# Performance work log

Measured on AMD Instinct MI355X. Metric: run time of the kernel, lower is better.

## Reference

```python
import jax, jax.numpy as jnp
import numpy as np

SUBSET_CHANNELS = 128


def setup_inputs() -> dict:
    key = jax.random.key(0)
    k_in, k_q, k_k, k_v = jax.random.split(key, 4)
    B, S, C, D = 8, 2048, 1024, SUBSET_CHANNELS
    scale = 1.0 / np.sqrt(C)  # ~ default torch Linear init scale
    return {
        "input": jax.random.normal(k_in, (B, S, C), dtype=jnp.float32),
        "Wq": jax.random.normal(k_q, (C, D), dtype=jnp.float32) * scale,
        "Wk": jax.random.normal(k_k, (C, D), dtype=jnp.float32) * scale,
        "Wv": jax.random.normal(k_v, (C, D), dtype=jnp.float32) * scale,
    }


def reference(input, Wq, Wk, Wv):
    # Projections (bias=False): [B,S,C] @ [C,D] -> [B,S,D]
    Q = input @ Wq
    K = input @ Wk
    V = input @ Wv
    D = Wq.shape[1]
    # scores[b, i, j] = Q[b,i,:] . K[b,j,:], scaled by sqrt(subset_channels)
    scores = jnp.einsum("bqd,bkd->bqk", Q, K) / jnp.sqrt(jnp.asarray(D, Q.dtype))
    # NOTE: original applies softmax over dim=1 (the QUERY axis), non-standard.
    att = jax.nn.softmax(scores, axis=1)
    # output[b, i, :] = sum_j att[b,i,j] * V[b,j,:]
    return jnp.einsum("bqk,bkd->bqd", att, V)
```

## Files before the change

### kernel.cpp

```cpp
#include <hip/hip_runtime.h>
#include <hip/hip_bf16.h>

typedef __bf16 bf16_t;
typedef bf16_t bf16x4 __attribute__((ext_vector_type(4)));
typedef bf16_t bf16x8 __attribute__((ext_vector_type(8)));
typedef float f32x4 __attribute__((ext_vector_type(4)));
typedef __attribute__((address_space(1))) const unsigned int gu32_t;
typedef __attribute__((address_space(3))) unsigned int lu32_t;

#define MFMA(a, b, c) __builtin_amdgcn_mfma_f32_16x16x32_bf16(a, b, c, 0, 0, 0)

constexpr int B = 8, S = 2048, C = 1024, D = 128;
constexpr float C2 = 0.12751744f;


__global__ __launch_bounds__(256) void k_wt(const float* Wq, const float* Wk, const float* Wv, bf16_t* Wf) {
    int ct = blockIdx.x, w = blockIdx.y;
    const float* src = (w == 0) ? Wq : ((w == 1) ? Wk : Wv);
    __shared__ bf16_t tile[16][132];
    int t = threadIdx.x;
    int cr = t >> 4, dq = t & 15;
    const float* p = src + (size_t)(ct * 16 + cr) * D + dq * 8;
    f32x4 v0 = *(const f32x4*)p;
    f32x4 v1 = *(const f32x4*)(p + 4);
#pragma unroll
    for (int q = 0; q < 4; ++q) { tile[cr][dq * 8 + q] = (bf16_t)v0[q]; tile[cr][dq * 8 + 4 + q] = (bf16_t)v1[q]; }
    __syncthreads();
    int n = t >> 1, g = t & 1;
    bf16x8 o;
#pragma unroll
    for (int cc = 0; cc < 8; ++cc) o[cc] = tile[g * 8 + cc][n];
    int c8 = ct * 2 + g;
    int nblk = w * 8 + (n >> 4);
    size_t a = ((size_t)(nblk * 32 + (c8 >> 2)) * 64 + (c8 & 3) * 16 + (n & 15)) * 8;
    *(bf16x8*)(Wf + a) = o;
}

__global__ __launch_bounds__(512, 4) void k_qkv(const float* X, const bf16_t* Wf,
                                                bf16_t* Qf, bf16_t* Kf, float* Vf,
                                                float* Out) {
    __shared__ __align__(16) char pool_[65536];
    bf16_t* xfr = (bf16_t*)pool_;
    bf16_t* qkL = (bf16_t*)pool_;
    float*  vL  = (float*)(pool_ + 16896);
    int mt = blockIdx.x;
    int t = threadIdx.x;
    int lane = t & 63, wid = t >> 6;
    int lr = lane & 15, lg = lane >> 4;
    int rw = mt * 32;

    {
        f32x4* O4 = (f32x4*)Out;
        f32x4 z = {};
        int u = mt * 512 + t;
        __builtin_nontemporal_store(z, O4 + u);
        __builtin_nontemporal_store(z, O4 + u + 262144);
    }

    {
        f32x4 xa[8], xb[8];
#pragma unroll
        for (int p = 0; p < 8; ++p) {
            int fi = p * 8 + wid;
            int m = rw + (fi >> 5) * 16 + lr;
            int c = (fi & 31) * 32 + lg * 8;
            const f32x4* px = (const f32x4*)(X + (size_t)m * C + c);
            xa[p] = __builtin_nontemporal_load(px);
            xb[p] = __builtin_nontemporal_load(px + 1);
        }
#pragma unroll
        for (int p = 0; p < 8; ++p) {
            bf16x8 o;
#pragma unroll
            for (int q = 0; q < 4; ++q) { o[q] = (bf16_t)xa[p][q]; o[4 + q] = (bf16_t)xb[p][q]; }
            *(bf16x8*)&xfr[(size_t)(p * 8 + wid) * 512 + lane * 8] = o;
        }
    }

    f32x4 acc[2][3] = {};
    const bf16_t* wbase = Wf + (size_t)(wid * 3) * 32 * 512 + lane * 8;
    auto wld = [&](int nf, int kkg) {
        return *(const bf16x8*)(wbase + (size_t)(nf * 32 + kkg) * 512);
    };

    bf16x8 wr_[3][3];
#pragma unroll
    for (int d = 0; d < 3; ++d)
#pragma unroll
        for (int nf = 0; nf < 3; ++nf) wr_[d][nf] = wld(nf, d);
    __syncthreads();

#pragma unroll
    for (int kk = 0; kk < 32; ++kk) {
        int slot = kk % 3;
        bf16x8 a0 = *(const bf16x8*)&xfr[(size_t)kk * 512 + lane * 8];
        bf16x8 a1 = *(const bf16x8*)&xfr[(size_t)(32 + kk) * 512 + lane * 8];
        __builtin_amdgcn_s_setprio(1);
        acc[0][0] = MFMA(a0, wr_[slot][0], acc[0][0]);
        acc[1][0] = MFMA(a1, wr_[slot][0], acc[1][0]);
        acc[0][1] = MFMA(a0, wr_[slot][1], acc[0][1]);
        acc[1][1] = MFMA(a1, wr_[slot][1], acc[1][1]);
        acc[0][2] = MFMA(a0, wr_[slot][2], acc[0][2]);
        acc[1][2] = MFMA(a1, wr_[slot][2], acc[1][2]);
        __builtin_amdgcn_s_setprio(0);
        if (kk < 29) {
#pragma unroll
            for (int nf = 0; nf < 3; ++nf) wr_[slot][nf] = wld(nf, kk + 3);
        }
    }

    __syncthreads();
#pragma unroll
    for (int mi = 0; mi < 2; ++mi)
#pragma unroll
        for (int nf = 0; nf < 3; ++nf) {
            int n = wid * 48 + nf * 16 + lr;
            int sel = (wid * 48 + nf * 16) >> 7;
#pragma unroll
            for (int r = 0; r < 4; ++r) {
                int mloc = mi * 16 + lg * 4 + r;
                float v = acc[mi][nf][r];
                if (sel == 2) vL[mloc * 132 + (n - 256)] = v;
                else          qkL[mloc * 264 + n] = (bf16_t)v;
            }
        }
    __syncthreads();
#pragma unroll
    for (int p = 0; p < 2; ++p) {
        int F = wid * 2 + p;
        int isK = F >> 3, iblk = (F >> 2) & 1, dblk = F & 3;
        int m16 = lane & 15, kg = lane >> 4;
        int col = isK * 128 + dblk * 32 + kg * 8;
        bf16x8 o = *(const bf16x8*)&qkL[(iblk * 16 + m16) * 264 + col];
        bf16_t* dst = isK ? Kf : Qf;
        size_t frg = (size_t)((rw >> 4) + iblk) * 4 + dblk;
        __builtin_nontemporal_store(o, (bf16x8*)(dst + (frg * 64 + lane) * 8));
    }
#pragma unroll
    for (int p = 0; p < 2; ++p) {
        int u = p * 512 + t;
        int m = u >> 5, dq = u & 31;
        f32x4 v = *(const f32x4*)&vL[m * 132 + dq * 4];
        __builtin_nontemporal_store(v, (f32x4*)(Vf + (size_t)(rw + m) * D + dq * 4));
    }
}

__global__ __launch_bounds__(512, 4) void k_sum(const bf16_t* Qf, const bf16_t* Kf,
                                                const float* Vf, bf16_t* Vt2) {
    int l = blockIdx.x;
    int b = l & 7, jt = l >> 3;
    int j0 = jt * 32;
    int t = threadIdx.x;
    int lane = t & 63, wid = t >> 6;
    __shared__ __align__(16) bf16_t vtile[128 * 40];
    __shared__ float lsum[256];
    __shared__ float linv[32];

    bf16x8 kf[2][4];
    int jblkg = (b * S + j0) >> 4;
#pragma unroll
    for (int jF = 0; jF < 2; ++jF)
#pragma unroll
        for (int kk = 0; kk < 4; ++kk)
            kf[jF][kk] = *(const bf16x8*)(Kf + ((size_t)((jblkg + jF) * 4 + kk) * 64 + lane) * 8);

    float ls0 = 0.f, ls1 = 0.f;
#pragma unroll 4
    for (int tt = 0; tt < 16; ++tt) {
        int iblk = (b * S + wid * 256 + tt * 16) >> 4;
        bf16x8 qa[4];
#pragma unroll
        for (int kk = 0; kk < 4; ++kk)
            qa[kk] = *(const bf16x8*)(Qf + ((size_t)(iblk * 4 + kk) * 64 + lane) * 8);
        f32x4 s0 = {}, s1 = {};
#pragma unroll
        for (int kk = 0; kk < 4; ++kk) {
            s0 = MFMA(qa[kk], kf[0][kk], s0);
            s1 = MFMA(qa[kk], kf[1][kk], s1);
        }
#pragma unroll
        for (int r = 0; r < 4; ++r) { ls0 += exp2f(s0[r] * C2); ls1 += exp2f(s1[r] * C2); }
    }
    {
        float v0 = ls0 + __shfl_xor(ls0, 16); v0 += __shfl_xor(v0, 32);
        float v1 = ls1 + __shfl_xor(ls1, 16); v1 += __shfl_xor(v1, 32);
        if (lane < 16) { lsum[wid * 32 + lane] = v0; lsum[wid * 32 + 16 + lane] = v1; }
    }
    __syncthreads();
    if (t < 32) {
        float ss = 0.f;
#pragma unroll
        for (int w = 0; w < 8; ++w) ss += lsum[w * 32 + t];
        linv[t] = 1.0f / ss;
    }
    __syncthreads();
#pragma unroll
    for (int p = 0; p < 2; ++p) {
        int u = p * 512 + t;
        int jj = u & 31, dq = u >> 5;
        f32x4 v = *(const f32x4*)(Vf + (size_t)(b * S + j0 + jj) * D + dq * 4);
        float inv = linv[jj];
#pragma unroll
        for (int q = 0; q < 4; ++q)
            vtile[(dq * 4 + q) * 40 + jj] = (bf16_t)(v[q] * inv);
    }
    __syncthreads();
    {
        int d = t >> 2, jg = t & 3;
        bf16x8 row = *(const bf16x8*)&vtile[d * 40 + jg * 8];
        size_t j32g = (size_t)b * 64 + jt;
        size_t a = ((j32g * 8 + (d >> 4)) * 64 + jg * 16 + (d & 15)) * 8;
        *(bf16x8*)(Vt2 + a) = row;
    }
}

__global__ __launch_bounds__(512, 4) void k_out(const bf16_t* Qf, const bf16_t* Kf,
                                                const bf16_t* Vt2, float* Out) {
    int l = blockIdx.x;
    int b = l & 7, it = (l >> 3) & 31, jh = l >> 8;
    int ibase = it * 64;
    int t = threadIdx.x;
    int lane = t & 63, wid = t >> 6;
    int lr = lane & 15, lg = lane >> 4;
    int ig = wid >> 1, jq = wid & 1;
    __shared__ __align__(16) bf16_t pool[37888];
    bf16_t* klds = pool;
    bf16_t* vlds = pool + 16384;
    bf16_t* pl = pool + 32768 + wid * 640;

    bf16x8 qf[4];
    int iblk = (b * S + ibase + ig * 16) >> 4;
#pragma unroll
    for (int kk = 0; kk < 4; ++kk)
        qf[kk] = *(const bf16x8*)(Qf + ((size_t)(iblk * 4 + kk) * 64 + lane) * 8);

    f32x4 acc[8] = {};
    const bf16_t* kbase = Kf + (size_t)(b * S + jh * 1024) * 128 + wid * 1024 + lane * 8;
    const bf16_t* vbase = Vt2 + (size_t)(b * 64 + jh * 32) * 4096 + wid * 1024 + lane * 8;

    auto stageKV = [&](int bufi, int tt) {
        const bf16_t* gk = kbase + (size_t)tt * 8192;
        __builtin_amdgcn_global_load_lds((gu32_t*)gk, (lu32_t*)&klds[bufi * 8192 + wid * 1024], 16, 0, 0);
        __builtin_amdgcn_global_load_lds((gu32_t*)(gk + 512), (lu32_t*)&klds[bufi * 8192 + wid * 1024 + 512], 16, 0, 0);
        const bf16_t* gv = vbase + (size_t)tt * 8192;
        __builtin_amdgcn_global_load_lds((gu32_t*)gv, (lu32_t*)&vlds[bufi * 8192 + wid * 1024], 16, 0, 0);
        __builtin_amdgcn_global_load_lds((gu32_t*)(gv + 512), (lu32_t*)&vlds[bufi * 8192 + wid * 1024 + 512], 16, 0, 0);
    };
    stageKV(0, 0);
    __syncthreads();

    for (int tt = 0; tt < 16; ++tt) {
        int buf = tt & 1;
        if (tt < 15) stageKV(buf ^ 1, tt + 1);
#pragma unroll
        for (int jF = 0; jF < 2; ++jF) {
            const bf16_t* kl = &klds[buf * 8192 + ((jq * 2 + jF) * 4) * 512 + lane * 8];
            f32x4 s = {};
            s = MFMA(*(const bf16x8*)(kl), qf[0], s);
            s = MFMA(*(const bf16x8*)(kl + 512), qf[1], s);
            s = MFMA(*(const bf16x8*)(kl + 1024), qf[2], s);
            s = MFMA(*(const bf16x8*)(kl + 1536), qf[3], s);
            bf16x4 pv;
#pragma unroll
            for (int r = 0; r < 4; ++r) pv[r] = (bf16_t)exp2f(s[r] * C2);
            *(bf16x4*)&pl[lr * 40 + jF * 16 + lg * 4] = pv;
        }
        bf16x8 pa = *(const bf16x8*)&pl[lr * 40 + lg * 8];
        const bf16_t* vl = &vlds[buf * 8192 + jq * 4096 + lane * 8];
        __builtin_amdgcn_s_setprio(1);
#pragma unroll
        for (int dc = 0; dc < 8; ++dc)
            acc[dc] = MFMA(pa, *(const bf16x8*)(vl + dc * 512), acc[dc]);
        __builtin_amdgcn_s_setprio(0);
        __syncthreads();
    }

    float* R = (float*)pool + ig * 2048;
    if (jq == 1) {
#pragma unroll
        for (int dc = 0; dc < 8; ++dc)
#pragma unroll
            for (int r = 0; r < 4; ++r)
                R[(lg * 4 + r) * 128 + dc * 16 + lr] = acc[dc][r];
    }
    __syncthreads();
    if (jq == 0) {
#pragma unroll
        for (int dc = 0; dc < 8; ++dc)
#pragma unroll
            for (int r = 0; r < 4; ++r)
                atomicAdd(&Out[(size_t)(b * S + ibase + ig * 16 + lg * 4 + r) * 128 + dc * 16 + lr],
                          acc[dc][r] + R[(lg * 4 + r) * 128 + dc * 16 + lr]);
    }
}

extern "C" void kernel_launch(void* const* d_in, const int* in_sizes, int n_in,
                              void* d_out, int out_size, void* d_ws, size_t ws_size,
                              hipStream_t stream) {
    const float* X  = (const float*)d_in[0];
    const float* Wq = (const float*)d_in[1];
    const float* Wk = (const float*)d_in[2];
    const float* Wv = (const float*)d_in[3];
    char* ws = (char*)d_ws;
    bf16_t* Wf  = (bf16_t*)(ws);
    bf16_t* Qf  = (bf16_t*)(ws + (1ull << 20));
    bf16_t* Kf  = (bf16_t*)(ws + (5ull << 20));
    float*  Vf  = (float*)(ws + (9ull << 20));
    bf16_t* Vt2 = (bf16_t*)(ws + (17ull << 20));
    float* Out = (float*)d_out;

    k_wt<<<dim3(64, 3), dim3(256), 0, stream>>>(Wq, Wk, Wv, Wf);
    k_qkv<<<dim3(512), dim3(512), 0, stream>>>(X, Wf, Qf, Kf, Vf, Out);
    k_sum<<<dim3(512), dim3(512), 0, stream>>>(Qf, Kf, Vf, Vt2);
    k_out<<<dim3(512), dim3(512), 0, stream>>>(Qf, Kf, Vt2, Out);
}
```

Baseline: 95.29 us.

## Pipeline X loading in QKV projection and restructure attention output kernel tiling

The QKV projection kernel now streams X in four K-chunks through a double-buffered LDS region instead of loading all of it up front. This halves shared memory and overlaps global loads with MFMA work. The output kernel drops LDS staging of K/V and the cross-wave reduction. Each wave now handles 32 query rows over a quarter of the keys, reading K and V fragments directly from global memory and atomically adding into the output, with a grid half the size. This raises register reuse of each K/V fragment across two query blocks, but relies on cache hits for repeated global fragment loads and doubles the per-wave accumulator registers.

```diff
diff --git a/kernel.cpp b/kernel.cpp
--- a/kernel.cpp
+++ b/kernel.cpp
@@ -5,8 +5,6 @@
 typedef bf16_t bf16x4 __attribute__((ext_vector_type(4)));
 typedef bf16_t bf16x8 __attribute__((ext_vector_type(8)));
 typedef float f32x4 __attribute__((ext_vector_type(4)));
-typedef __attribute__((address_space(1))) const unsigned int gu32_t;
-typedef __attribute__((address_space(3))) unsigned int lu32_t;
 
 #define MFMA(a, b, c) __builtin_amdgcn_mfma_f32_16x16x32_bf16(a, b, c, 0, 0, 0)
 
@@ -39,7 +37,7 @@
 __global__ __launch_bounds__(512, 4) void k_qkv(const float* X, const bf16_t* Wf,
                                                 bf16_t* Qf, bf16_t* Kf, float* Vf,
                                                 float* Out) {
-    __shared__ __align__(16) char pool_[65536];
+    __shared__ __align__(16) char pool_[33792];
     bf16_t* xfr = (bf16_t*)pool_;
     bf16_t* qkL = (bf16_t*)pool_;
     float*  vL  = (float*)(pool_ + 16896);
@@ -57,25 +55,26 @@
         __builtin_nontemporal_store(z, O4 + u + 262144);
     }
 
-    {
-        f32x4 xa[8], xb[8];
-#pragma unroll
-        for (int p = 0; p < 8; ++p) {
+    auto loadX = [&](f32x4* xr, int c) {
+#pragma unroll
+        for (int p = 0; p < 2; ++p) {
             int fi = p * 8 + wid;
-            int m = rw + (fi >> 5) * 16 + lr;
-            int c = (fi & 31) * 32 + lg * 8;
-            const f32x4* px = (const f32x4*)(X + (size_t)m * C + c);
-            xa[p] = __builtin_nontemporal_load(px);
-            xb[p] = __builtin_nontemporal_load(px + 1);
-        }
-#pragma unroll
-        for (int p = 0; p < 8; ++p) {
+            int m = rw + (fi >> 3) * 16 + lr;
+            int k = c * 256 + (fi & 7) * 32 + lg * 8;
+            const f32x4* px = (const f32x4*)(X + (size_t)m * C + k);
+            xr[p * 2]     = __builtin_nontemporal_load(px);
+            xr[p * 2 + 1] = __builtin_nontemporal_load(px + 1);
+        }
+    };
+    auto writeX = [&](const f32x4* xr, int buf) {
+#pragma unroll
+        for (int p = 0; p < 2; ++p) {
             bf16x8 o;
 #pragma unroll
-            for (int q = 0; q < 4; ++q) { o[q] = (bf16_t)xa[p][q]; o[4 + q] = (bf16_t)xb[p][q]; }
-            *(bf16x8*)&xfr[(size_t)(p * 8 + wid) * 512 + lane * 8] = o;
-        }
-    }
+            for (int q = 0; q < 4; ++q) { o[q] = (bf16_t)xr[p * 2][q]; o[4 + q] = (bf16_t)xr[p * 2 + 1][q]; }
+            *(bf16x8*)&xfr[(size_t)buf * 8192 + (size_t)(p * 8 + wid) * 512 + lane * 8] = o;
+        }
+    };
 
     f32x4 acc[2][3] = {};
     const bf16_t* wbase = Wf + (size_t)(wid * 3) * 32 * 512 + lane * 8;
@@ -83,33 +82,41 @@
         return *(const bf16x8*)(wbase + (size_t)(nf * 32 + kkg) * 512);
     };
 
-    bf16x8 wr_[3][3];
-#pragma unroll
-    for (int d = 0; d < 3; ++d)
-#pragma unroll
-        for (int nf = 0; nf < 3; ++nf) wr_[d][nf] = wld(nf, d);
-    __syncthreads();
-
-#pragma unroll
-    for (int kk = 0; kk < 32; ++kk) {
-        int slot = kk % 3;
-        bf16x8 a0 = *(const bf16x8*)&xfr[(size_t)kk * 512 + lane * 8];
-        bf16x8 a1 = *(const bf16x8*)&xfr[(size_t)(32 + kk) * 512 + lane * 8];
-        __builtin_amdgcn_s_setprio(1);
-        acc[0][0] = MFMA(a0, wr_[slot][0], acc[0][0]);
-        acc[1][0] = MFMA(a1, wr_[slot][0], acc[1][0]);
-        acc[0][1] = MFMA(a0, wr_[slot][1], acc[0][1]);
-        acc[1][1] = MFMA(a1, wr_[slot][1], acc[1][1]);
-        acc[0][2] = MFMA(a0, wr_[slot][2], acc[0][2]);
-        acc[1][2] = MFMA(a1, wr_[slot][2], acc[1][2]);
-        __builtin_amdgcn_s_setprio(0);
-        if (kk < 29) {
-#pragma unroll
-            for (int nf = 0; nf < 3; ++nf) wr_[slot][nf] = wld(nf, kk + 3);
-        }
-    }
-
-    __syncthreads();
+    f32x4 xr[4];
+    loadX(xr, 0);
+    bf16x8 wb[2][3];
+#pragma unroll
+    for (int nf = 0; nf < 3; ++nf) { wb[0][nf] = wld(nf, 0); wb[1][nf] = wld(nf, 1); }
+    writeX(xr, 0);
+    __syncthreads();
+
+#pragma unroll
+    for (int c = 0; c < 4; ++c) {
+        if (c < 3) loadX(xr, c + 1);
+        int buf = c & 1;
+#pragma unroll
+        for (int kk = 0; kk < 8; ++kk) {
+            int kkg = c * 8 + kk;
+            int sl = kkg & 1;
+            bf16x8 a0 = *(const bf16x8*)&xfr[(size_t)buf * 8192 + (size_t)kk * 512 + lane * 8];
+            bf16x8 a1 = *(const bf16x8*)&xfr[(size_t)buf * 8192 + (size_t)(8 + kk) * 512 + lane * 8];
+            __builtin_amdgcn_s_setprio(1);
+            acc[0][0] = MFMA(a0, wb[sl][0], acc[0][0]);
+            acc[1][0] = MFMA(a1, wb[sl][0], acc[1][0]);
+            acc[0][1] = MFMA(a0, wb[sl][1], acc[0][1]);
+            acc[1][1] = MFMA(a1, wb[sl][1], acc[1][1]);
+            acc[0][2] = MFMA(a0, wb[sl][2], acc[0][2]);
+            acc[1][2] = MFMA(a1, wb[sl][2], acc[1][2]);
+            __builtin_amdgcn_s_setprio(0);
+            if (kkg < 30) {
+#pragma unroll
+                for (int nf = 0; nf < 3; ++nf) wb[sl][nf] = wld(nf, kkg + 2);
+            }
+        }
+        if (c < 3) writeX(xr, (c + 1) & 1);
+        __syncthreads();
+    }
+
 #pragma unroll
     for (int mi = 0; mi < 2; ++mi)
 #pragma unroll
@@ -214,84 +221,70 @@
     }
 }
 
-__global__ __launch_bounds__(512, 4) void k_out(const bf16_t* Qf, const bf16_t* Kf,
+__global__ __launch_bounds__(512, 2) void k_out(const bf16_t* Qf, const bf16_t* Kf,
                                                 const bf16_t* Vt2, float* Out) {
     int l = blockIdx.x;
-    int b = l & 7, it = (l >> 3) & 31, jh = l >> 8;
-    int ibase = it * 64;
+    int b = l & 7, it = (l >> 3) & 7, jq = l >> 6;
     int t = threadIdx.x;
     int lane = t & 63, wid = t >> 6;
     int lr = lane & 15, lg = lane >> 4;
-    int ig = wid >> 1, jq = wid & 1;
-    __shared__ __align__(16) bf16_t pool[37888];
-    bf16_t* klds = pool;
-    bf16_t* vlds = pool + 16384;
-    bf16_t* pl = pool + 32768 + wid * 640;
-
-    bf16x8 qf[4];
-    int iblk = (b * S + ibase + ig * 16) >> 4;
-#pragma unroll
-    for (int kk = 0; kk < 4; ++kk)
-        qf[kk] = *(const bf16x8*)(Qf + ((size_t)(iblk * 4 + kk) * 64 + lane) * 8);
-
-    f32x4 acc[8] = {};
-    const bf16_t* kbase = Kf + (size_t)(b * S + jh * 1024) * 128 + wid * 1024 + lane * 8;
-    const bf16_t* vbase = Vt2 + (size_t)(b * 64 + jh * 32) * 4096 + wid * 1024 + lane * 8;
-
-    auto stageKV = [&](int bufi, int tt) {
-        const bf16_t* gk = kbase + (size_t)tt * 8192;
-        __builtin_amdgcn_global_load_lds((gu32_t*)gk, (lu32_t*)&klds[bufi * 8192 + wid * 1024], 16, 0, 0);
-        __builtin_amdgcn_global_load_lds((gu32_t*)(gk + 512), (lu32_t*)&klds[bufi * 8192 + wid * 1024 + 512], 16, 0, 0);
-        const bf16_t* gv = vbase + (size_t)tt * 8192;
-        __builtin_amdgcn_global_load_lds((gu32_t*)gv, (lu32_t*)&vlds[bufi * 8192 + wid * 1024], 16, 0, 0);
-        __builtin_amdgcn_global_load_lds((gu32_t*)(gv + 512), (lu32_t*)&vlds[bufi * 8192 + wid * 1024 + 512], 16, 0, 0);
-    };
-    stageKV(0, 0);
-    __syncthreads();
-
+    __shared__ __align__(16) bf16_t pl_all[8][1280];
+    bf16_t* pl = pl_all[wid];
+    int ibase0 = it * 256 + wid * 32;
+
+    bf16x8 qf[2][4];
+    int iblk = (b * S + ibase0) >> 4;
+#pragma unroll
+    for (int iF = 0; iF < 2; ++iF)
+#pragma unroll
+        for (int kk = 0; kk < 4; ++kk)
+            qf[iF][kk] = *(const bf16x8*)(Qf + ((size_t)((iblk + iF) * 4 + kk) * 64 + lane) * 8);
+
+    f32x4 acc[2][8] = {};
+    int jblk0 = b * 128 + jq * 32;
+
+#pragma unroll 4
     for (int tt = 0; tt < 16; ++tt) {
-        int buf = tt & 1;
-        if (tt < 15) stageKV(buf ^ 1, tt + 1);
-#pragma unroll
-        for (int jF = 0; jF < 2; ++jF) {
-            const bf16_t* kl = &klds[buf * 8192 + ((jq * 2 + jF) * 4) * 512 + lane * 8];
-            f32x4 s = {};
-            s = MFMA(*(const bf16x8*)(kl), qf[0], s);
-            s = MFMA(*(const bf16x8*)(kl + 512), qf[1], s);
-            s = MFMA(*(const bf16x8*)(kl + 1024), qf[2], s);
-            s = MFMA(*(const bf16x8*)(kl + 1536), qf[3], s);
-            bf16x4 pv;
-#pragma unroll
-            for (int r = 0; r < 4; ++r) pv[r] = (bf16_t)exp2f(s[r] * C2);
-            *(bf16x4*)&pl[lr * 40 + jF * 16 + lg * 4] = pv;
-        }
-        bf16x8 pa = *(const bf16x8*)&pl[lr * 40 + lg * 8];
-        const bf16_t* vl = &vlds[buf * 8192 + jq * 4096 + lane * 8];
+        bf16x8 kf[2][4];
+#pragma unroll
+        for (int jF = 0; jF < 2; ++jF)
+#pragma unroll
+            for (int kk = 0; kk < 4; ++kk)
+                kf[jF][kk] = *(const bf16x8*)(Kf + ((size_t)((jblk0 + tt * 2 + jF) * 4 + kk) * 64 + lane) * 8);
+#pragma unroll
+        for (int jF = 0; jF < 2; ++jF)
+#pragma unroll
+            for (int iF = 0; iF < 2; ++iF) {
+                f32x4 s = {};
+                s = MFMA(kf[jF][0], qf[iF][0], s);
+                s = MFMA(kf[jF][1], qf[iF][1], s);
+                s = MFMA(kf[jF][2], qf[iF][2], s);
+                s = MFMA(kf[jF][3], qf[iF][3], s);
+                bf16x4 pv;
+#pragma unroll
+                for (int r = 0; r < 4; ++r) pv[r] = (bf16_t)exp2f(s[r] * C2);
+                *(bf16x4*)&pl[(iF * 16 + lr) * 40 + jF * 16 + lg * 4] = pv;
+            }
+        bf16x8 pa0 = *(const bf16x8*)&pl[lr * 40 + lg * 8];
+        bf16x8 pa1 = *(const bf16x8*)&pl[(16 + lr) * 40 + lg * 8];
         __builtin_amdgcn_s_setprio(1);
 #pragma unroll
+        for (int dc = 0; dc < 8; ++dc) {
+            bf16x8 vv = *(const bf16x8*)(Vt2 + ((size_t)((b * 64 + jq * 16 + tt) * 8 + dc) * 64 + lane) * 8);
+            acc[0][dc] = MFMA(pa0, vv, acc[0][dc]);
+            acc[1][dc] = MFMA(pa1, vv, acc[1][dc]);
+        }
+        __builtin_amdgcn_s_setprio(0);
+    }
+
+#pragma unroll
+    for (int iF = 0; iF < 2; ++iF)
+#pragma unroll
         for (int dc = 0; dc < 8; ++dc)
-            acc[dc] = MFMA(pa, *(const bf16x8*)(vl + dc * 512), acc[dc]);
-        __builtin_amdgcn_s_setprio(0);
-        __syncthreads();
-    }
-
-    float* R = (float*)pool + ig * 2048;
-    if (jq == 1) {
-#pragma unroll
-        for (int dc = 0; dc < 8; ++dc)
 #pragma unroll
             for (int r = 0; r < 4; ++r)
-                R[(lg * 4 + r) * 128 + dc * 16 + lr] = acc[dc][r];
-    }
-    __syncthreads();
-    if (jq == 0) {
-#pragma unroll
-        for (int dc = 0; dc < 8; ++dc)
-#pragma unroll
-            for (int r = 0; r < 4; ++r)
-                atomicAdd(&Out[(size_t)(b * S + ibase + ig * 16 + lg * 4 + r) * 128 + dc * 16 + lr],
-                          acc[dc][r] + R[(lg * 4 + r) * 128 + dc * 16 + lr]);
-    }
+                atomicAdd(&Out[(size_t)(b * S + ibase0 + iF * 16 + lg * 4 + r) * 128 + dc * 16 + lr],
+                          acc[iF][dc][r]);
 }
 
 extern "C" void kernel_launch(void* const* d_in, const int* in_sizes, int n_in,
@@ -312,5 +305,5 @@
     k_wt<<<dim3(64, 3), dim3(256), 0, stream>>>(Wq, Wk, Wv, Wf);
     k_qkv<<<dim3(512), dim3(512), 0, stream>>>(X, Wf, Qf, Kf, Vf, Out);
     k_sum<<<dim3(512), dim3(512), 0, stream>>>(Qf, Kf, Vf, Vt2);
-    k_out<<<dim3(512), dim3(512), 0, stream>>>(Qf, Kf, Vt2, Out);
-}
+    k_out<<<dim3(256), dim3(512), 0, stream>>>(Qf, Kf, Vt2, Out);
+}
```

New measurement: 109.6 us. +15.0%, slower.

## Materialize softmax numerators in column-sum pass instead of recomputing in output pass

Applied to the files above, without the earlier changes.

The column-sum kernel now writes the bf16 exponentiated scores into a global buffer in MFMA fragment layout while accumulating column sums. The output kernel becomes a plain P·V GEMM reading that buffer and the scaled V, dropping the QK^T recompute, exp work and LDS staging. This trades redundant compute for a large extra write and read of the full attention matrix through HBM.

```diff
diff --git a/kernel.cpp b/kernel.cpp
--- a/kernel.cpp
+++ b/kernel.cpp
@@ -5,8 +5,6 @@
 typedef bf16_t bf16x4 __attribute__((ext_vector_type(4)));
 typedef bf16_t bf16x8 __attribute__((ext_vector_type(8)));
 typedef float f32x4 __attribute__((ext_vector_type(4)));
-typedef __attribute__((address_space(1))) const unsigned int gu32_t;
-typedef __attribute__((address_space(3))) unsigned int lu32_t;
 
 #define MFMA(a, b, c) __builtin_amdgcn_mfma_f32_16x16x32_bf16(a, b, c, 0, 0, 0)
 
@@ -145,16 +143,19 @@
     }
 }
 
-__global__ __launch_bounds__(512, 4) void k_sum(const bf16_t* Qf, const bf16_t* Kf,
-                                                const float* Vf, bf16_t* Vt2) {
+__global__ __launch_bounds__(512, 4) void k_sp(const bf16_t* Qf, const bf16_t* Kf,
+                                               const float* Vf, bf16_t* Vt2, bf16_t* Pf) {
     int l = blockIdx.x;
     int b = l & 7, jt = l >> 3;
     int j0 = jt * 32;
     int t = threadIdx.x;
     int lane = t & 63, wid = t >> 6;
+    int lr = lane & 15, lg = lane >> 4;
     __shared__ __align__(16) bf16_t vtile[128 * 40];
+    __shared__ __align__(16) bf16_t pl_all[8][1280];
     __shared__ float lsum[256];
     __shared__ float linv[32];
+    bf16_t* pl = pl_all[wid];
 
     bf16x8 kf[2][4];
     int jblkg = (b * S + j0) >> 4;
@@ -164,7 +165,9 @@
         for (int kk = 0; kk < 4; ++kk)
             kf[jF][kk] = *(const bf16x8*)(Kf + ((size_t)((jblkg + jF) * 4 + kk) * 64 + lane) * 8);
 
-    float ls0 = 0.f, ls1 = 0.f;
+    float ls[2][4] = {};
+    bf16_t* pbase = Pf + ((size_t)(b * 128 + wid * 16) * 64 + jt) * 512 + lane * 8;
+
 #pragma unroll 4
     for (int tt = 0; tt < 16; ++tt) {
         int iblk = (b * S + wid * 256 + tt * 16) >> 4;
@@ -172,20 +175,34 @@
 #pragma unroll
         for (int kk = 0; kk < 4; ++kk)
             qa[kk] = *(const bf16x8*)(Qf + ((size_t)(iblk * 4 + kk) * 64 + lane) * 8);
-        f32x4 s0 = {}, s1 = {};
-#pragma unroll
-        for (int kk = 0; kk < 4; ++kk) {
-            s0 = MFMA(qa[kk], kf[0][kk], s0);
-            s1 = MFMA(qa[kk], kf[1][kk], s1);
-        }
-#pragma unroll
-        for (int r = 0; r < 4; ++r) { ls0 += exp2f(s0[r] * C2); ls1 += exp2f(s1[r] * C2); }
-    }
-    {
-        float v0 = ls0 + __shfl_xor(ls0, 16); v0 += __shfl_xor(v0, 32);
-        float v1 = ls1 + __shfl_xor(ls1, 16); v1 += __shfl_xor(v1, 32);
-        if (lane < 16) { lsum[wid * 32 + lane] = v0; lsum[wid * 32 + 16 + lane] = v1; }
-    }
+#pragma unroll
+        for (int jF = 0; jF < 2; ++jF) {
+            f32x4 s = {};
+            s = MFMA(kf[jF][0], qa[0], s);
+            s = MFMA(kf[jF][1], qa[1], s);
+            s = MFMA(kf[jF][2], qa[2], s);
+            s = MFMA(kf[jF][3], qa[3], s);
+            bf16x4 pv;
+#pragma unroll
+            for (int r = 0; r < 4; ++r) {
+                float e = exp2f(s[r] * C2);
+                ls[jF][r] += e;
+                pv[r] = (bf16_t)e;
+            }
+            *(bf16x4*)&pl[lr * 40 + jF * 16 + lg * 4] = pv;
+        }
+        bf16x8 pa = *(const bf16x8*)&pl[lr * 40 + lg * 8];
+        __builtin_nontemporal_store(pa, (bf16x8*)(pbase + (size_t)tt * 64 * 512));
+    }
+#pragma unroll
+    for (int jF = 0; jF < 2; ++jF)
+#pragma unroll
+        for (int r = 0; r < 4; ++r) {
+            float v = ls[jF][r];
+            v += __shfl_xor(v, 1); v += __shfl_xor(v, 2);
+            v += __shfl_xor(v, 4); v += __shfl_xor(v, 8);
+            if (lr == 0) lsum[wid * 32 + jF * 16 + lg * 4 + r] = v;
+        }
     __syncthreads();
     if (t < 32) {
         float ss = 0.f;
@@ -214,84 +231,38 @@
     }
 }
 
-__global__ __launch_bounds__(512, 4) void k_out(const bf16_t* Qf, const bf16_t* Kf,
-                                                const bf16_t* Vt2, float* Out) {
+__global__ __launch_bounds__(512, 4) void k_out2(const bf16_t* Pf, const bf16_t* Vt2,
+                                                 float* Out) {
     int l = blockIdx.x;
     int b = l & 7, it = (l >> 3) & 31, jh = l >> 8;
-    int ibase = it * 64;
     int t = threadIdx.x;
     int lane = t & 63, wid = t >> 6;
     int lr = lane & 15, lg = lane >> 4;
-    int ig = wid >> 1, jq = wid & 1;
-    __shared__ __align__(16) bf16_t pool[37888];
-    bf16_t* klds = pool;
-    bf16_t* vlds = pool + 16384;
-    bf16_t* pl = pool + 32768 + wid * 640;
-
-    bf16x8 qf[4];
-    int iblk = (b * S + ibase + ig * 16) >> 4;
-#pragma unroll
-    for (int kk = 0; kk < 4; ++kk)
-        qf[kk] = *(const bf16x8*)(Qf + ((size_t)(iblk * 4 + kk) * 64 + lane) * 8);
-
-    f32x4 acc[8] = {};
-    const bf16_t* kbase = Kf + (size_t)(b * S + jh * 1024) * 128 + wid * 1024 + lane * 8;
-    const bf16_t* vbase = Vt2 + (size_t)(b * 64 + jh * 32) * 4096 + wid * 1024 + lane * 8;
-
-    auto stageKV = [&](int bufi, int tt) {
-        const bf16_t* gk = kbase + (size_t)tt * 8192;
-        __builtin_amdgcn_global_load_lds((gu32_t*)gk, (lu32_t*)&klds[bufi * 8192 + wid * 1024], 16, 0, 0);
-        __builtin_amdgcn_global_load_lds((gu32_t*)(gk + 512), (lu32_t*)&klds[bufi * 8192 + wid * 1024 + 512], 16, 0, 0);
-        const bf16_t* gv = vbase + (size_t)tt * 8192;
-        __builtin_amdgcn_global_load_lds((gu32_t*)gv, (lu32_t*)&vlds[bufi * 8192 + wid * 1024], 16, 0, 0);
-        __builtin_amdgcn_global_load_lds((gu32_t*)(gv + 512), (lu32_t*)&vlds[bufi * 8192 + wid * 1024 + 512], 16, 0, 0);
-    };
-    stageKV(0, 0);
-    __syncthreads();
-
-    for (int tt = 0; tt < 16; ++tt) {
-        int buf = tt & 1;
-        if (tt < 15) stageKV(buf ^ 1, tt + 1);
-#pragma unroll
-        for (int jF = 0; jF < 2; ++jF) {
-            const bf16_t* kl = &klds[buf * 8192 + ((jq * 2 + jF) * 4) * 512 + lane * 8];
-            f32x4 s = {};
-            s = MFMA(*(const bf16x8*)(kl), qf[0], s);
-            s = MFMA(*(const bf16x8*)(kl + 512), qf[1], s);
-            s = MFMA(*(const bf16x8*)(kl + 1024), qf[2], s);
-            s = MFMA(*(const bf16x8*)(kl + 1536), qf[3], s);
-            bf16x4 pv;
-#pragma unroll
-            for (int r = 0; r < 4; ++r) pv[r] = (bf16_t)exp2f(s[r] * C2);
-            *(bf16x4*)&pl[lr * 40 + jF * 16 + lg * 4] = pv;
-        }
-        bf16x8 pa = *(const bf16x8*)&pl[lr * 40 + lg * 8];
-        const bf16_t* vl = &vlds[buf * 8192 + jq * 4096 + lane * 8];
+    int wib = wid >> 1, dh = wid & 1;
+
+    f32x4 acc[4] = {};
+    const bf16_t* abase = Pf + (((size_t)(b * 128 + it * 4 + wib) * 64) + jh * 32) * 512 + lane * 8;
+    const bf16_t* vbase = Vt2 + ((size_t)((b * 64 + jh * 32) * 8 + dh * 4) * 64 + lane) * 8;
+
+#pragma unroll 4
+    for (int ks = 0; ks < 32; ++ks) {
+        bf16x8 pa = *(const bf16x8*)(abase + (size_t)ks * 512);
+        const bf16_t* vp = vbase + (size_t)ks * 8 * 512;
         __builtin_amdgcn_s_setprio(1);
 #pragma unroll
-        for (int dc = 0; dc < 8; ++dc)
-            acc[dc] = MFMA(pa, *(const bf16x8*)(vl + dc * 512), acc[dc]);
+        for (int dc = 0; dc < 4; ++dc) {
+            bf16x8 vv = *(const bf16x8*)(vp + (size_t)dc * 512);
+            acc[dc] = MFMA(pa, vv, acc[dc]);
+        }
         __builtin_amdgcn_s_setprio(0);
-        __syncthreads();
-    }
-
-    float* R = (float*)pool + ig * 2048;
-    if (jq == 1) {
-#pragma unroll
-        for (int dc = 0; dc < 8; ++dc)
-#pragma unroll
-            for (int r = 0; r < 4; ++r)
-                R[(lg * 4 + r) * 128 + dc * 16 + lr] = acc[dc][r];
-    }
-    __syncthreads();
-    if (jq == 0) {
-#pragma unroll
-        for (int dc = 0; dc < 8; ++dc)
-#pragma unroll
-            for (int r = 0; r < 4; ++r)
-                atomicAdd(&Out[(size_t)(b * S + ibase + ig * 16 + lg * 4 + r) * 128 + dc * 16 + lr],
-                          acc[dc][r] + R[(lg * 4 + r) * 128 + dc * 16 + lr]);
-    }
+    }
+
+#pragma unroll
+    for (int dc = 0; dc < 4; ++dc)
+#pragma unroll
+        for (int r = 0; r < 4; ++r)
+            atomicAdd(&Out[(size_t)(b * S + (it * 4 + wib) * 16 + lg * 4 + r) * 128 + dh * 64 + dc * 16 + lr],
+                      acc[dc][r]);
 }
 
 extern "C" void kernel_launch(void* const* d_in, const int* in_sizes, int n_in,
@@ -307,10 +278,11 @@
     bf16_t* Kf  = (bf16_t*)(ws + (5ull << 20));
     float*  Vf  = (float*)(ws + (9ull << 20));
     bf16_t* Vt2 = (bf16_t*)(ws + (17ull << 20));
+    bf16_t* Pf  = (bf16_t*)(ws + (32ull << 20));
     float* Out = (float*)d_out;
 
     k_wt<<<dim3(64, 3), dim3(256), 0, stream>>>(Wq, Wk, Wv, Wf);
     k_qkv<<<dim3(512), dim3(512), 0, stream>>>(X, Wf, Qf, Kf, Vf, Out);
-    k_sum<<<dim3(512), dim3(512), 0, stream>>>(Qf, Kf, Vf, Vt2);
-    k_out<<<dim3(512), dim3(512), 0, stream>>>(Qf, Kf, Vt2, Out);
-}
+    k_sp<<<dim3(512), dim3(512), 0, stream>>>(Qf, Kf, Vf, Vt2, Pf);
+    k_out2<<<dim3(512), dim3(512), 0, stream>>>(Pf, Vt2, Out);
+}
```

Measured after the change: 116.4 us. +22.2%, slower.

## Split attention over full key range per block, drop atomics and zero-init

Applied to the files above, without the earlier changes.

Replaces the output kernel: each block now covers 64 query rows for one batch and walks all 2048 keys, with each wave taking a quarter of the keys and two 16-row query tiles. This removes the split over key halves, so the atomicAdd accumulation and the zeroing of Out in the projection kernel go away and the output is written with plain stores after an in-LDS tree reduction across waves. K and V fragments are now read straight from global memory instead of being double-buffered into LDS with global_load_lds. The grid halves to 256 blocks, and the extra syncs for the reduction and the reliance on cache for K/V reuse may cost some occupancy and latency hiding.

```diff
diff --git a/kernel.cpp b/kernel.cpp
--- a/kernel.cpp
+++ b/kernel.cpp
@@ -5,8 +5,6 @@
 typedef bf16_t bf16x4 __attribute__((ext_vector_type(4)));
 typedef bf16_t bf16x8 __attribute__((ext_vector_type(8)));
 typedef float f32x4 __attribute__((ext_vector_type(4)));
-typedef __attribute__((address_space(1))) const unsigned int gu32_t;
-typedef __attribute__((address_space(3))) unsigned int lu32_t;
 
 #define MFMA(a, b, c) __builtin_amdgcn_mfma_f32_16x16x32_bf16(a, b, c, 0, 0, 0)
 
@@ -37,8 +35,7 @@
 }
 
 __global__ __launch_bounds__(512, 4) void k_qkv(const float* X, const bf16_t* Wf,
-                                                bf16_t* Qf, bf16_t* Kf, float* Vf,
-                                                float* Out) {
+                                                bf16_t* Qf, bf16_t* Kf, float* Vf) {
     __shared__ __align__(16) char pool_[65536];
     bf16_t* xfr = (bf16_t*)pool_;
     bf16_t* qkL = (bf16_t*)pool_;
@@ -48,14 +45,6 @@
     int lane = t & 63, wid = t >> 6;
     int lr = lane & 15, lg = lane >> 4;
     int rw = mt * 32;
-
-    {
-        f32x4* O4 = (f32x4*)Out;
-        f32x4 z = {};
-        int u = mt * 512 + t;
-        __builtin_nontemporal_store(z, O4 + u);
-        __builtin_nontemporal_store(z, O4 + u + 262144);
-    }
 
     {
         f32x4 xa[8], xb[8];
@@ -214,83 +203,104 @@
     }
 }
 
-__global__ __launch_bounds__(512, 4) void k_out(const bf16_t* Qf, const bf16_t* Kf,
+__global__ __launch_bounds__(512, 2) void k_att(const bf16_t* Qf, const bf16_t* Kf,
                                                 const bf16_t* Vt2, float* Out) {
     int l = blockIdx.x;
-    int b = l & 7, it = (l >> 3) & 31, jh = l >> 8;
-    int ibase = it * 64;
+    int b = l & 7, g = l >> 3;
     int t = threadIdx.x;
     int lane = t & 63, wid = t >> 6;
     int lr = lane & 15, lg = lane >> 4;
-    int ig = wid >> 1, jq = wid & 1;
-    __shared__ __align__(16) bf16_t pool[37888];
-    bf16_t* klds = pool;
-    bf16_t* vlds = pool + 16384;
-    bf16_t* pl = pool + 32768 + wid * 640;
-
-    bf16x8 qf[4];
-    int iblk = (b * S + ibase + ig * 16) >> 4;
-#pragma unroll
-    for (int kk = 0; kk < 4; ++kk)
-        qf[kk] = *(const bf16x8*)(Qf + ((size_t)(iblk * 4 + kk) * 64 + lane) * 8);
-
-    f32x4 acc[8] = {};
-    const bf16_t* kbase = Kf + (size_t)(b * S + jh * 1024) * 128 + wid * 1024 + lane * 8;
-    const bf16_t* vbase = Vt2 + (size_t)(b * 64 + jh * 32) * 4096 + wid * 1024 + lane * 8;
-
-    auto stageKV = [&](int bufi, int tt) {
-        const bf16_t* gk = kbase + (size_t)tt * 8192;
-        __builtin_amdgcn_global_load_lds((gu32_t*)gk, (lu32_t*)&klds[bufi * 8192 + wid * 1024], 16, 0, 0);
-        __builtin_amdgcn_global_load_lds((gu32_t*)(gk + 512), (lu32_t*)&klds[bufi * 8192 + wid * 1024 + 512], 16, 0, 0);
-        const bf16_t* gv = vbase + (size_t)tt * 8192;
-        __builtin_amdgcn_global_load_lds((gu32_t*)gv, (lu32_t*)&vlds[bufi * 8192 + wid * 1024], 16, 0, 0);
-        __builtin_amdgcn_global_load_lds((gu32_t*)(gv + 512), (lu32_t*)&vlds[bufi * 8192 + wid * 1024 + 512], 16, 0, 0);
+    int iun = wid >> 2, jq = wid & 3;
+    int iu = g * 2 + iun;
+    __shared__ __align__(16) char pool_[33792];
+    bf16_t* pl = (bf16_t*)pool_ + wid * 1280;
+    float* Ru = (float*)pool_ + iun * 4224;
+
+    bf16x8 qa[2][4];
+    int iblkg = (b * S + iu * 32) >> 4;
+#pragma unroll
+    for (int ib = 0; ib < 2; ++ib)
+#pragma unroll
+        for (int kk = 0; kk < 4; ++kk)
+            qa[ib][kk] = *(const bf16x8*)(Qf + ((size_t)((iblkg + ib) * 4 + kk) * 64 + lane) * 8);
+
+    f32x4 acc[2][8] = {};
+    int jb0 = b * 128 + jq * 32;
+    int jv0 = b * 64 + jq * 16;
+
+#pragma unroll 2
+    for (int tt = 0; tt < 16; ++tt) {
+#pragma unroll
+        for (int jF = 0; jF < 2; ++jF) {
+            bf16x8 kf[4];
+#pragma unroll
+            for (int kk = 0; kk < 4; ++kk)
+                kf[kk] = *(const bf16x8*)(Kf + ((size_t)((jb0 + tt * 2 + jF) * 4 + kk) * 64 + lane) * 8);
+#pragma unroll
+            for (int ib = 0; ib < 2; ++ib) {
+                f32x4 s = {};
+                s = MFMA(kf[0], qa[ib][0], s);
+                s = MFMA(kf[1], qa[ib][1], s);
+                s = MFMA(kf[2], qa[ib][2], s);
+                s = MFMA(kf[3], qa[ib][3], s);
+                bf16x4 pv;
+#pragma unroll
+                for (int r = 0; r < 4; ++r) pv[r] = (bf16_t)exp2f(s[r] * C2);
+                *(bf16x4*)&pl[(ib * 16 + lr) * 40 + jF * 16 + lg * 4] = pv;
+            }
+        }
+        bf16x8 pa0 = *(const bf16x8*)&pl[lr * 40 + lg * 8];
+        bf16x8 pa1 = *(const bf16x8*)&pl[(16 + lr) * 40 + lg * 8];
+        const bf16_t* vp = Vt2 + ((size_t)(jv0 + tt) * 8 * 64) * 8 + (size_t)lane * 8;
+        __builtin_amdgcn_s_setprio(1);
+#pragma unroll
+        for (int dc = 0; dc < 8; ++dc) {
+            bf16x8 vv = *(const bf16x8*)(vp + (size_t)dc * 512);
+            acc[0][dc] = MFMA(pa0, vv, acc[0][dc]);
+            acc[1][dc] = MFMA(pa1, vv, acc[1][dc]);
+        }
+        __builtin_amdgcn_s_setprio(0);
+    }
+
+    auto wrR = [&]() {
+#pragma unroll
+        for (int ib = 0; ib < 2; ++ib)
+#pragma unroll
+            for (int dc = 0; dc < 8; ++dc)
+#pragma unroll
+                for (int r = 0; r < 4; ++r)
+                    Ru[(ib * 16 + lg * 4 + r) * 132 + dc * 16 + lr] = acc[ib][dc][r];
     };
-    stageKV(0, 0);
-    __syncthreads();
-
-    for (int tt = 0; tt < 16; ++tt) {
-        int buf = tt & 1;
-        if (tt < 15) stageKV(buf ^ 1, tt + 1);
-#pragma unroll
-        for (int jF = 0; jF < 2; ++jF) {
-            const bf16_t* kl = &klds[buf * 8192 + ((jq * 2 + jF) * 4) * 512 + lane * 8];
-            f32x4 s = {};
-            s = MFMA(*(const bf16x8*)(kl), qf[0], s);
-            s = MFMA(*(const bf16x8*)(kl + 512), qf[1], s);
-            s = MFMA(*(const bf16x8*)(kl + 1024), qf[2], s);
-            s = MFMA(*(const bf16x8*)(kl + 1536), qf[3], s);
-            bf16x4 pv;
-#pragma unroll
-            for (int r = 0; r < 4; ++r) pv[r] = (bf16_t)exp2f(s[r] * C2);
-            *(bf16x4*)&pl[lr * 40 + jF * 16 + lg * 4] = pv;
-        }
-        bf16x8 pa = *(const bf16x8*)&pl[lr * 40 + lg * 8];
-        const bf16_t* vl = &vlds[buf * 8192 + jq * 4096 + lane * 8];
-        __builtin_amdgcn_s_setprio(1);
-#pragma unroll
-        for (int dc = 0; dc < 8; ++dc)
-            acc[dc] = MFMA(pa, *(const bf16x8*)(vl + dc * 512), acc[dc]);
-        __builtin_amdgcn_s_setprio(0);
-        __syncthreads();
-    }
-
-    float* R = (float*)pool + ig * 2048;
-    if (jq == 1) {
-#pragma unroll
-        for (int dc = 0; dc < 8; ++dc)
-#pragma unroll
-            for (int r = 0; r < 4; ++r)
-                R[(lg * 4 + r) * 128 + dc * 16 + lr] = acc[dc][r];
-    }
+    auto adR = [&]() {
+#pragma unroll
+        for (int ib = 0; ib < 2; ++ib)
+#pragma unroll
+            for (int dc = 0; dc < 8; ++dc)
+#pragma unroll
+                for (int r = 0; r < 4; ++r)
+                    acc[ib][dc][r] += Ru[(ib * 16 + lg * 4 + r) * 132 + dc * 16 + lr];
+    };
+    __syncthreads();
+    if (jq == 1) wrR();
+    __syncthreads();
+    if (jq == 0) adR();
+    __syncthreads();
+    if (jq == 3) wrR();
+    __syncthreads();
+    if (jq == 2) adR();
+    __syncthreads();
+    if (jq == 2) wrR();
     __syncthreads();
     if (jq == 0) {
-#pragma unroll
-        for (int dc = 0; dc < 8; ++dc)
-#pragma unroll
-            for (int r = 0; r < 4; ++r)
-                atomicAdd(&Out[(size_t)(b * S + ibase + ig * 16 + lg * 4 + r) * 128 + dc * 16 + lr],
-                          acc[dc][r] + R[(lg * 4 + r) * 128 + dc * 16 + lr]);
+        adR();
+#pragma unroll
+        for (int ib = 0; ib < 2; ++ib)
+#pragma unroll
+            for (int dc = 0; dc < 8; ++dc)
+#pragma unroll
+                for (int r = 0; r < 4; ++r)
+                    __builtin_nontemporal_store(acc[ib][dc][r],
+                        &Out[(size_t)(b * S + iu * 32 + ib * 16 + lg * 4 + r) * 128 + dc * 16 + lr]);
     }
 }
 
@@ -310,7 +320,7 @@
     float* Out = (float*)d_out;
 
     k_wt<<<dim3(64, 3), dim3(256), 0, stream>>>(Wq, Wk, Wv, Wf);
-    k_qkv<<<dim3(512), dim3(512), 0, stream>>>(X, Wf, Qf, Kf, Vf, Out);
+    k_qkv<<<dim3(512), dim3(512), 0, stream>>>(X, Wf, Qf, Kf, Vf);
     k_sum<<<dim3(512), dim3(512), 0, stream>>>(Qf, Kf, Vf, Vt2);
-    k_out<<<dim3(512), dim3(512), 0, stream>>>(Qf, Kf, Vt2, Out);
-}
+    k_att<<<dim3(256), dim3(512), 0, stream>>>(Qf, Kf, Vt2, Out);
+}
```

New measurement: 88.42 us. -7.2%, faster.
